# Kernel optimization log

Hardware: AMD Instinct MI355X
Metric: run time of the kernel (lower is better)

The kernel has to match this reference:

```python
import jax, jax.numpy as jnp
import numpy as np

C = 512
H = 8  # num_heads
GROUPS = 32
EPS = 1e-5


def group_norm(x, scale, bias):
    # x: [b, c, h, w]; GroupNorm(32, c) normalizes over (c//32, h, w) per group
    b, c, h, w = x.shape
    xg = x.reshape(b, GROUPS, c // GROUPS * h * w)
    mean = jnp.mean(xg, axis=-1, keepdims=True)
    var = jnp.var(xg, axis=-1, keepdims=True)
    xg = (xg - mean) * jax.lax.rsqrt(var + EPS)
    x = xg.reshape(b, c, h, w)
    return x * scale[None, :, None, None] + bias[None, :, None, None]


def setup_inputs() -> dict:
    key = jax.random.key(0)
    ks = jax.random.split(key, 6)
    init = 0.02
    return {
        "x": jax.random.normal(ks[0], (8, C, 32, 32), dtype=jnp.float32),
        "gn_scale": jnp.ones((C,), jnp.float32),
        "gn_bias": jnp.zeros((C,), jnp.float32),
        "Wq": jax.random.normal(ks[1], (C, C), jnp.float32) * init,
        "bq": jnp.zeros((C,), jnp.float32),
        "Wk": jax.random.normal(ks[2], (C, C), jnp.float32) * init,
        "bk": jnp.zeros((C,), jnp.float32),
        "Wv": jax.random.normal(ks[3], (C, C), jnp.float32) * init,
        "bv": jnp.zeros((C,), jnp.float32),
        "Wo": jax.random.normal(ks[4], (C, C), jnp.float32) * init,
        "bo": jnp.zeros((C,), jnp.float32),
    }


def reference(x, gn_scale, gn_bias, Wq, bq, Wk, bk, Wv, bv, Wo, bo):
    b, c, h, w = x.shape
    s = h * w  # number of spatial tokens
    d = c // H  # head dim
    residual = x
    xn = group_norm(x, gn_scale, gn_bias)
    t = xn.reshape(b, c, s).transpose(0, 2, 1)  # [b, s, c]
    # torch Linear: y = x @ W.T + b
    q = t @ Wq.T + bq
    k = t @ Wk.T + bk
    v = t @ Wv.T + bv
    q = q.reshape(b, s, H, d).transpose(0, 2, 1, 3)  # [b, H, s, d]
    k = k.reshape(b, s, H, d).transpose(0, 2, 1, 3)
    v = v.reshape(b, s, H, d).transpose(0, 2, 1, 3)
    scale = d ** -0.5
    attn = jnp.einsum('bhqd,bhkd->bhqk', q, k) * scale  # [b, H, s, s]
    attn = jax.nn.softmax(attn, axis=-1)
    out = jnp.einsum('bhqk,bhkd->bhqd', attn, v)  # [b, H, s, d]
    out = out.transpose(0, 2, 1, 3).reshape(b, s, c)
    out = out @ Wo.T + bo
    out = out.transpose(0, 2, 1).reshape(b, c, h, w)
    return out + residual
```

## Files before the change

kernel.cpp:

```cpp
#include <hip/hip_runtime.h>


typedef __bf16 bf16x8 __attribute__((ext_vector_type(8)));
typedef __bf16 bf16x4 __attribute__((ext_vector_type(4)));
typedef float floatx4 __attribute__((ext_vector_type(4)));

static __device__ __forceinline__ floatx4 mfma16(bf16x8 a, bf16x8 b, floatx4 c) {
  return __builtin_amdgcn_mfma_f32_16x16x32_bf16(a, b, c, 0, 0, 0);
}
static __device__ __forceinline__ floatx4 mfma_fp8(long a, long b, floatx4 c) {
  return __builtin_amdgcn_mfma_f32_16x16x32_fp8_fp8(a, b, c, 0, 0, 0);
}

static __device__ __forceinline__ void async_cp16(const void* g, void* l) {
  __builtin_amdgcn_global_load_lds(
      (const __attribute__((address_space(1))) unsigned int*)g,
      (__attribute__((address_space(3))) unsigned int*)l, 16, 0, 0);
}

static __device__ __forceinline__ uint2 cvt8_bf16_fp8(uint4 v) {
  union { uint4 u; __bf16 h[8]; } in; in.u = v;
  float f[8];
#pragma unroll
  for (int i = 0; i < 8; ++i) f[i] = (float)in.h[i];
  int lo = __builtin_amdgcn_cvt_pk_fp8_f32(f[0], f[1], 0, false);
  lo = __builtin_amdgcn_cvt_pk_fp8_f32(f[2], f[3], lo, true);
  int hi = __builtin_amdgcn_cvt_pk_fp8_f32(f[4], f[5], 0, false);
  hi = __builtin_amdgcn_cvt_pk_fp8_f32(f[6], f[7], hi, true);
  return uint2{(unsigned)lo, (unsigned)hi};
}

__global__ __launch_bounds__(256) void prep_gn_kernel(
    const float* __restrict__ x, const float* __restrict__ gamma,
    const float* __restrict__ beta,
    const float* __restrict__ Wq, const float* __restrict__ bq,
    const float* __restrict__ Wk, const float* __restrict__ bk,
    const float* __restrict__ Wv, const float* __restrict__ bv,
    const float* __restrict__ Wo,
    __bf16* __restrict__ wqkv, __bf16* __restrict__ wo,
    float* __restrict__ bqkv, __bf16* __restrict__ t) {
  __shared__ __bf16 tile[16 * 1024];
  __shared__ float rbuf[8];
  int tid = threadIdx.x;
  int bx = blockIdx.x;

  if (bx >= 256) {
    const float SC = 0.125f * 1.4426950408889634f;
    int i = ((bx - 256) * 256 + tid) * 4;
    float4 q4 = *(const float4*)(Wq + i);
    float4 k4 = *(const float4*)(Wk + i);
    float4 v4 = *(const float4*)(Wv + i);
    float4 o4 = *(const float4*)(Wo + i);
    *(bf16x4*)(wqkv + i) = (bf16x4){(__bf16)(q4.x * SC), (__bf16)(q4.y * SC),
                                    (__bf16)(q4.z * SC), (__bf16)(q4.w * SC)};
    *(bf16x4*)(wqkv + 262144 + i) =
        (bf16x4){(__bf16)k4.x, (__bf16)k4.y, (__bf16)k4.z, (__bf16)k4.w};
    *(bf16x4*)(wqkv + 524288 + i) =
        (bf16x4){(__bf16)v4.x, (__bf16)v4.y, (__bf16)v4.z, (__bf16)v4.w};
    *(bf16x4*)(wo + i) =
        (bf16x4){(__bf16)o4.x, (__bf16)o4.y, (__bf16)o4.z, (__bf16)o4.w};
    int j = (bx - 256) * 256 + tid;
    if (j < 512) {
      bqkv[j]        = bq[j] * SC;
      bqkv[512 + j]  = bk[j];
      bqkv[1024 + j] = bv[j];
    }
    return;
  }

  int b = bx >> 5, g = bx & 31;
  const float* xp = x + (size_t)(b * 512 + g * 16) * 1024;
  const float4* xp4 = (const float4*)xp;

  float sacc = 0.f, ssacc = 0.f;
#pragma unroll
  for (int it = 0; it < 16; ++it) {
    float4 v = xp4[it * 256 + tid];
    sacc += v.x + v.y + v.z + v.w;
    ssacc += v.x * v.x + v.y * v.y + v.z * v.z + v.w * v.w;
  }
#pragma unroll
  for (int off = 1; off < 64; off <<= 1) {
    sacc += __shfl_xor(sacc, off);
    ssacc += __shfl_xor(ssacc, off);
  }
  int wv = tid >> 6;
  if ((tid & 63) == 0) { rbuf[wv] = sacc; rbuf[4 + wv] = ssacc; }
  __syncthreads();
  float S1 = rbuf[0] + rbuf[1] + rbuf[2] + rbuf[3];
  float S2 = rbuf[4] + rbuf[5] + rbuf[6] + rbuf[7];
  float mean = S1 * (1.f / 16384.f);
  float var = S2 * (1.f / 16384.f) - mean * mean;
  float inv = rsqrtf(var + 1e-5f);

#pragma unroll
  for (int it = 0; it < 16; ++it) {
    float4 v = xp4[it * 256 + tid];
    float ga = gamma[g * 16 + it], be = beta[g * 16 + it];
    int base = it * 1024 + tid * 4;
    tile[base + 0] = (__bf16)((v.x - mean) * inv * ga + be);
    tile[base + 1] = (__bf16)((v.y - mean) * inv * ga + be);
    tile[base + 2] = (__bf16)((v.z - mean) * inv * ga + be);
    tile[base + 3] = (__bf16)((v.w - mean) * inv * ga + be);
  }
  __syncthreads();

#pragma unroll
  for (int j = 0; j < 8; ++j) {
    int qid = j * 256 + tid;
    int sidx = qid >> 1, half = qid & 1;
    union { uint4 u; __bf16 h[8]; } o;
#pragma unroll
    for (int i = 0; i < 8; ++i) o.h[i] = tile[(half * 8 + i) * 1024 + sidx];
    *(uint4*)(t + (size_t)(b * 1024 + sidx) * 512 + g * 16 + half * 8) = o.u;
  }
}

__global__ __launch_bounds__(256) void gemm_qkv_kernel(
    const __bf16* __restrict__ t, const __bf16* __restrict__ wqkv,
    const float* __restrict__ bqkv,
    unsigned char* __restrict__ qb, unsigned char* __restrict__ kb,
    unsigned char* __restrict__ vt) {
  __shared__ __align__(16) __bf16 smem[8192];
  __bf16* As = smem;
  __bf16* Bs = smem + 4096;
  int tid = threadIdx.x;
  int m0 = blockIdx.x * 128;
  int n0 = blockIdx.y * 128;
  int wave = tid >> 6, lane = tid & 63;
  int l15 = lane & 15, quad = lane >> 4;
  int wm = wave >> 1, wn = wave & 1;

  floatx4 acc[4][4];
#pragma unroll
  for (int mi = 0; mi < 4; ++mi)
#pragma unroll
    for (int ni = 0; ni < 4; ++ni) acc[mi][ni] = (floatx4){0.f, 0.f, 0.f, 0.f};

  int r1 = tid >> 2, o1 = (tid & 3) * 8;
  const __bf16* gA1 = t + (size_t)(m0 + r1) * 512 + o1;
  const __bf16* gA2 = t + (size_t)(m0 + 64 + r1) * 512 + o1;
  const __bf16* gB1 = wqkv + (size_t)(n0 + r1) * 512 + o1;
  const __bf16* gB2 = wqkv + (size_t)(n0 + 64 + r1) * 512 + o1;
  __bf16* lA1 = As + tid * 8;
  __bf16* lA2 = As + 2048 + tid * 8;
  __bf16* lB1 = Bs + tid * 8;
  __bf16* lB2 = Bs + 2048 + tid * 8;

  for (int k0 = 0; k0 < 512; k0 += 32) {
    async_cp16(gA1 + k0, lA1);
    async_cp16(gA2 + k0, lA2);
    async_cp16(gB1 + k0, lB1);
    async_cp16(gB2 + k0, lB2);
    __syncthreads();
    bf16x8 af[4], bfr[4];
#pragma unroll
    for (int mi = 0; mi < 4; ++mi)
      af[mi] = *(const bf16x8*)&As[(wm * 64 + mi * 16 + l15) * 32 + quad * 8];
#pragma unroll
    for (int ni = 0; ni < 4; ++ni)
      bfr[ni] = *(const bf16x8*)&Bs[(wn * 64 + ni * 16 + l15) * 32 + quad * 8];
#pragma unroll
    for (int mi = 0; mi < 4; ++mi)
#pragma unroll
      for (int ni = 0; ni < 4; ++ni)
        acc[mi][ni] = mfma16(af[mi], bfr[ni], acc[mi][ni]);
    __syncthreads();
  }

  int mat = n0 >> 9;
  int bidx = m0 >> 10, s0 = m0 & 1023;
  int hA = (n0 & 511) >> 6;
  float bias[4];
#pragma unroll
  for (int ni = 0; ni < 4; ++ni)
    bias[ni] = bqkv[n0 + wn * 64 + ni * 16 + l15];

  if (mat < 2) {
    unsigned char* dst = (mat == 0) ? qb : kb;
    for (int c = 0; c < 4; ++c) {
      if ((c >> 1) == wm) {
#pragma unroll
        for (int mi2 = 0; mi2 < 2; ++mi2) {
          int mi = (c & 1) * 2 + mi2;
          int lrow = mi2 * 16 + quad * 4;
#pragma unroll
          for (int ni = 0; ni < 4; ++ni)
#pragma unroll
            for (int r = 0; r < 4; ++r)
              smem[(lrow + r) * 136 + wn * 64 + ni * 16 + l15] =
                  (__bf16)(acc[mi][ni][r] + bias[ni]);
        }
      }
      __syncthreads();
#pragma unroll
      for (int u = 0; u < 2; ++u) {
        int f = tid * 16 + u * 8;
        int row = f >> 7, col = f & 127;
        uint2 val = cvt8_bf16_fp8(*(uint4*)&smem[row * 136 + col]);
        int head = hA + (col >> 6), d = col & 63;
        *(uint2*)(dst + ((size_t)(bidx * 8 + head) * 1024 + s0 + c * 32 + row) * 64 + d) = val;
      }
      __syncthreads();
    }
  } else {
    for (int c = 0; c < 4; ++c) {
      if ((c >> 1) == wn) {
#pragma unroll
        for (int ni2 = 0; ni2 < 2; ++ni2) {
          int ni = (c & 1) * 2 + ni2;
          int nrow = ni2 * 16 + l15;
#pragma unroll
          for (int mi = 0; mi < 4; ++mi)
#pragma unroll
            for (int r = 0; r < 4; ++r)
              smem[nrow * 136 + wm * 64 + mi * 16 + quad * 4 + r] =
                  (__bf16)(acc[mi][ni][r] + bias[ni]);
        }
      }
      __syncthreads();
#pragma unroll
      for (int u = 0; u < 2; ++u) {
        int f = tid * 16 + u * 8;
        int nrow = f >> 7, mcol = f & 127;
        uint2 val = cvt8_bf16_fp8(*(uint4*)&smem[nrow * 136 + mcol]);
        int nloc = c * 32 + nrow;
        int head = hA + (nloc >> 6), d = nloc & 63;
        *(uint2*)(vt + ((size_t)(bidx * 8 + head) * 64 + d) * 1024 + s0 + mcol) = val;
      }
      __syncthreads();
    }
  }
}

__global__ __launch_bounds__(256) void attn_kernel(
    const unsigned char* __restrict__ qb, const unsigned char* __restrict__ kb,
    const unsigned char* __restrict__ vt, __bf16* __restrict__ ao) {
  __shared__ __align__(16) unsigned char Ks[2][64 * 80];
  __shared__ __align__(16) unsigned char Vs[2][64 * 80];
  __shared__ __align__(16) __bf16 Ps[128 * 72];
  unsigned char* Psb = (unsigned char*)Ps;
  int tid = threadIdx.x;
  int bx = blockIdx.x;
  int b = bx >> 6, h = (bx >> 3) & 7, q128 = bx & 7;
  int wv = tid >> 6, lane = tid & 63, l15 = lane & 15, quad = lane >> 4;
  size_t bh = (size_t)(b * 8 + h) * 65536;
  const unsigned char* Qp = qb + bh;
  const unsigned char* Kp = kb + bh;
  const unsigned char* Vp = vt + bh;
  int q0 = q128 * 128, qw = q0 + wv * 32;

  long aq[2][2];
#pragma unroll
  for (int mi = 0; mi < 2; ++mi)
#pragma unroll
    for (int kh = 0; kh < 2; ++kh)
      aq[mi][kh] = *(const long*)(Qp + (size_t)(qw + mi * 16 + l15) * 64 + kh * 32 + quad * 8);

  const long ONES = 0x3838383838383838L;

  floatx4 oacc[2][4], lacc[2];
#pragma unroll
  for (int mi = 0; mi < 2; ++mi) {
    lacc[mi] = (floatx4){0.f, 0.f, 0.f, 0.f};
#pragma unroll
    for (int di = 0; di < 4; ++di) oacc[mi][di] = (floatx4){0.f, 0.f, 0.f, 0.f};
  }

  int srow = tid >> 2, scol = (tid & 3) * 16;
  int ldsoff = srow * 80 + scol;

  uint4 kr, vr;
  kr = *(const uint4*)(Kp + (size_t)srow * 64 + scol);
  vr = *(const uint4*)(Vp + (size_t)srow * 1024 + scol);

  for (int kt = 0; kt < 16; ++kt) {
    int cur = kt & 1;
    *(uint4*)&Ks[cur][ldsoff] = kr;
    *(uint4*)&Vs[cur][ldsoff] = vr;
    if (kt < 15) {
      int nt = kt + 1;
      kr = *(const uint4*)(Kp + (size_t)(nt * 64 + srow) * 64 + scol);
      vr = *(const uint4*)(Vp + (size_t)srow * 1024 + nt * 64 + scol);
    }
    __syncthreads();

    floatx4 sa[2][4];
#pragma unroll
    for (int ni = 0; ni < 4; ++ni) {
      long bk0 = *(const long*)&Ks[cur][(ni * 16 + l15) * 80 + quad * 8];
      long bk1 = *(const long*)&Ks[cur][(ni * 16 + l15) * 80 + 32 + quad * 8];
#pragma unroll
      for (int mi = 0; mi < 2; ++mi) {
        floatx4 s4 = (floatx4){0.f, 0.f, 0.f, 0.f};
        s4 = mfma_fp8(bk0, aq[mi][0], s4);
        s4 = mfma_fp8(bk1, aq[mi][1], s4);
        sa[mi][ni] = s4;
      }
    }

#pragma unroll
    for (int mi = 0; mi < 2; ++mi)
#pragma unroll
      for (int ni = 0; ni < 4; ++ni) {
        float e0 = __builtin_amdgcn_exp2f(sa[mi][ni][0]);
        float e1 = __builtin_amdgcn_exp2f(sa[mi][ni][1]);
        float e2 = __builtin_amdgcn_exp2f(sa[mi][ni][2]);
        float e3 = __builtin_amdgcn_exp2f(sa[mi][ni][3]);
        int pk = __builtin_amdgcn_cvt_pk_fp8_f32(e0, e1, 0, false);
        pk = __builtin_amdgcn_cvt_pk_fp8_f32(e2, e3, pk, true);
        *(unsigned int*)&Psb[(wv * 32 + mi * 16 + l15) * 72 + ni * 16 + quad * 4] =
            (unsigned)pk;
      }

    long ap[2][2];
#pragma unroll
    for (int mi = 0; mi < 2; ++mi) {
      ap[mi][0] = *(const long*)&Psb[(wv * 32 + mi * 16 + l15) * 72 + quad * 8];
      ap[mi][1] = *(const long*)&Psb[(wv * 32 + mi * 16 + l15) * 72 + 32 + quad * 8];
    }
#pragma unroll
    for (int di = 0; di < 4; ++di) {
      long bv0 = *(const long*)&Vs[cur][(di * 16 + l15) * 80 + quad * 8];
      long bv1 = *(const long*)&Vs[cur][(di * 16 + l15) * 80 + 32 + quad * 8];
#pragma unroll
      for (int mi = 0; mi < 2; ++mi) {
        oacc[mi][di] = mfma_fp8(ap[mi][0], bv0, oacc[mi][di]);
        oacc[mi][di] = mfma_fp8(ap[mi][1], bv1, oacc[mi][di]);
      }
    }
#pragma unroll
    for (int mi = 0; mi < 2; ++mi) {
      lacc[mi] = mfma_fp8(ap[mi][0], ONES, lacc[mi]);
      lacc[mi] = mfma_fp8(ap[mi][1], ONES, lacc[mi]);
    }
  }

  __syncthreads();
#pragma unroll
  for (int mi = 0; mi < 2; ++mi)
#pragma unroll
    for (int r = 0; r < 4; ++r) {
      float invl = 1.f / lacc[mi][r];
      int lrow = wv * 32 + mi * 16 + quad * 4 + r;
#pragma unroll
      for (int di = 0; di < 4; ++di)
        Ps[lrow * 72 + di * 16 + l15] = (__bf16)(oacc[mi][di][r] * invl);
    }
  __syncthreads();
  __bf16* aop = ao + (size_t)b * 524288 + h * 64;
#pragma unroll
  for (int u = 0; u < 4; ++u) {
    int idx = u * 256 + tid;
    int row = idx >> 3, col = (idx & 7) * 8;
    *(uint4*)(aop + (size_t)(q0 + row) * 512 + col) = *(uint4*)&Ps[row * 72 + col];
  }
}

__global__ __launch_bounds__(256) void gemm_out_kernel(
    const __bf16* __restrict__ ao, const __bf16* __restrict__ wo,
    const float* __restrict__ bo, const float* __restrict__ x,
    float* __restrict__ out) {
  __shared__ __align__(16) __bf16 As[128 * 32];
  __shared__ __align__(16) __bf16 Bs[64 * 32];
  __shared__ __align__(16) float ctile[32 * 132];
  int tid = threadIdx.x;
  int m0 = blockIdx.x * 128;
  int n0 = blockIdx.y * 64;
  int wave = tid >> 6, lane = tid & 63;
  int l15 = lane & 15, quad = lane >> 4;
  int wm = wave >> 1, wn = wave & 1;

  floatx4 acc[4][2];
#pragma unroll
  for (int mi = 0; mi < 4; ++mi)
#pragma unroll
    for (int ni = 0; ni < 2; ++ni) acc[mi][ni] = (floatx4){0.f, 0.f, 0.f, 0.f};

  int r1 = tid >> 2, o1 = (tid & 3) * 8;
  const __bf16* gA1 = ao + (size_t)(m0 + r1) * 512 + o1;
  const __bf16* gA2 = ao + (size_t)(m0 + 64 + r1) * 512 + o1;
  const __bf16* gB1 = wo + (size_t)(n0 + r1) * 512 + o1;
  __bf16* lA1 = As + tid * 8;
  __bf16* lA2 = As + 2048 + tid * 8;
  __bf16* lB1 = Bs + tid * 8;

  for (int k0 = 0; k0 < 512; k0 += 32) {
    async_cp16(gA1 + k0, lA1);
    async_cp16(gA2 + k0, lA2);
    async_cp16(gB1 + k0, lB1);
    __syncthreads();
    bf16x8 af[4], bfr[2];
#pragma unroll
    for (int mi = 0; mi < 4; ++mi)
      af[mi] = *(const bf16x8*)&As[(wm * 64 + mi * 16 + l15) * 32 + quad * 8];
#pragma unroll
    for (int ni = 0; ni < 2; ++ni)
      bfr[ni] = *(const bf16x8*)&Bs[(wn * 32 + ni * 16 + l15) * 32 + quad * 8];
#pragma unroll
    for (int mi = 0; mi < 4; ++mi)
#pragma unroll
      for (int ni = 0; ni < 2; ++ni)
        acc[mi][ni] = mfma16(af[mi], bfr[ni], acc[mi][ni]);
    __syncthreads();
  }

  int b = m0 >> 10, s0 = m0 & 1023;
  for (int cc = 0; cc < 2; ++cc) {
    __syncthreads();
    if (wn == cc) {
#pragma unroll
      for (int ni = 0; ni < 2; ++ni) {
        int nn = ni * 16 + l15;
        float bias = bo[n0 + cc * 32 + nn];
#pragma unroll
        for (int mi = 0; mi < 4; ++mi)
#pragma unroll
          for (int r = 0; r < 4; ++r)
            ctile[nn * 132 + wm * 64 + mi * 16 + quad * 4 + r] =
                acc[mi][ni][r] + bias;
      }
    }
    __syncthreads();
    int nn = tid >> 3, mlb = (tid & 7) * 16;
    int n = n0 + cc * 32 + nn;
    const float* xr = x + (size_t)(b * 512 + n) * 1024 + s0;
    float* orow = out + (size_t)(b * 512 + n) * 1024 + s0;
#pragma unroll
    for (int i = 0; i < 16; i += 4) {
      float4 cv = *(float4*)&ctile[nn * 132 + mlb + i];
      float4 xv = *(const float4*)&xr[mlb + i];
      float4 ov = {cv.x + xv.x, cv.y + xv.y, cv.z + xv.z, cv.w + xv.w};
      *(float4*)&orow[mlb + i] = ov;
    }
  }
}

extern "C" void kernel_launch(void* const* d_in, const int* in_sizes, int n_in,
                              void* d_out, int out_size, void* d_ws, size_t ws_size,
                              hipStream_t stream) {
  const float* x  = (const float*)d_in[0];
  const float* gs = (const float*)d_in[1];
  const float* gb = (const float*)d_in[2];
  const float* Wq = (const float*)d_in[3];
  const float* bq = (const float*)d_in[4];
  const float* Wk = (const float*)d_in[5];
  const float* bk = (const float*)d_in[6];
  const float* Wv = (const float*)d_in[7];
  const float* bv = (const float*)d_in[8];
  const float* Wo = (const float*)d_in[9];
  const float* bo = (const float*)d_in[10];
  float* out = (float*)d_out;

  char* ws = (char*)d_ws;
  __bf16* wqkv = (__bf16*)(ws);
  __bf16* wo   = (__bf16*)(ws + 1572864);
  float*  bqkv = (float*)(ws + 2097152);
  __bf16* t    = (__bf16*)(ws + 2103296);
  __bf16* ao   = t;
  unsigned char* qb = (unsigned char*)(ws + 10491904);
  unsigned char* kb = (unsigned char*)(ws + 14686208);
  unsigned char* vtb = (unsigned char*)(ws + 18880512);

  prep_gn_kernel<<<dim3(512), dim3(256), 0, stream>>>(
      x, gs, gb, Wq, bq, Wk, bk, Wv, bv, Wo, wqkv, wo, bqkv, t);
  gemm_qkv_kernel<<<dim3(64, 12), dim3(256), 0, stream>>>(t, wqkv, bqkv, qb, kb, vtb);
  attn_kernel<<<dim3(512), dim3(256), 0, stream>>>(qb, kb, vtb, ao);
  gemm_out_kernel<<<dim3(64, 8), dim3(256), 0, stream>>>(ao, wo, bo, x, out);
}
```

Before: 148.6 us.

## Switch QKV and output projection GEMMs to FP8 MFMA with swizzled LDS

Converts the normalized activations, the weights (scaled by 16) and the attention output to FP8, and runs both projection GEMMs with FP8 16x16x32 MFMA over a K-step of 64 using an XOR-swizzled LDS layout. The softmax scale moves from the Wq weights into the attention exp2 step, and the projection outputs are rescaled by 1/16 or 1/256. This halves the bytes moved for activations and weights and uses the faster FP8 matrix path, but adds more FP8 rounding error and extra conversion work in prep and attention.

Result: faster. 144.7 us (-2.7%).

```diff
diff --git a/kernel.cpp b/kernel.cpp
--- a/kernel.cpp
+++ b/kernel.cpp
@@ -5,9 +5,6 @@
 typedef __bf16 bf16x4 __attribute__((ext_vector_type(4)));
 typedef float floatx4 __attribute__((ext_vector_type(4)));
 
-static __device__ __forceinline__ floatx4 mfma16(bf16x8 a, bf16x8 b, floatx4 c) {
-  return __builtin_amdgcn_mfma_f32_16x16x32_bf16(a, b, c, 0, 0, 0);
-}
 static __device__ __forceinline__ floatx4 mfma_fp8(long a, long b, floatx4 c) {
   return __builtin_amdgcn_mfma_f32_16x16x32_fp8_fp8(a, b, c, 0, 0, 0);
 }
@@ -28,6 +25,14 @@
   int hi = __builtin_amdgcn_cvt_pk_fp8_f32(f[4], f[5], 0, false);
   hi = __builtin_amdgcn_cvt_pk_fp8_f32(f[6], f[7], hi, true);
   return uint2{(unsigned)lo, (unsigned)hi};
+}
+
+static __device__ __forceinline__ int swz_s(int r) {
+  return (r & 3) ^ ((r >> 2) & 3);
+}
+static __device__ __forceinline__ int frag_addr(int row, int kh, int quad) {
+  int chunk = (kh << 1) | (quad >> 1);
+  return row * 64 + ((chunk ^ swz_s(row)) << 4) + ((quad & 1) << 3);
 }
 
 __global__ __launch_bounds__(256) void prep_gn_kernel(
@@ -37,31 +42,35 @@
     const float* __restrict__ Wk, const float* __restrict__ bk,
     const float* __restrict__ Wv, const float* __restrict__ bv,
     const float* __restrict__ Wo,
-    __bf16* __restrict__ wqkv, __bf16* __restrict__ wo,
-    float* __restrict__ bqkv, __bf16* __restrict__ t) {
+    unsigned char* __restrict__ wqkv, unsigned char* __restrict__ wo,
+    float* __restrict__ bqkv, unsigned char* __restrict__ t) {
   __shared__ __bf16 tile[16 * 1024];
   __shared__ float rbuf[8];
   int tid = threadIdx.x;
   int bx = blockIdx.x;
 
   if (bx >= 256) {
-    const float SC = 0.125f * 1.4426950408889634f;
     int i = ((bx - 256) * 256 + tid) * 4;
     float4 q4 = *(const float4*)(Wq + i);
     float4 k4 = *(const float4*)(Wk + i);
     float4 v4 = *(const float4*)(Wv + i);
     float4 o4 = *(const float4*)(Wo + i);
-    *(bf16x4*)(wqkv + i) = (bf16x4){(__bf16)(q4.x * SC), (__bf16)(q4.y * SC),
-                                    (__bf16)(q4.z * SC), (__bf16)(q4.w * SC)};
-    *(bf16x4*)(wqkv + 262144 + i) =
-        (bf16x4){(__bf16)k4.x, (__bf16)k4.y, (__bf16)k4.z, (__bf16)k4.w};
-    *(bf16x4*)(wqkv + 524288 + i) =
-        (bf16x4){(__bf16)v4.x, (__bf16)v4.y, (__bf16)v4.z, (__bf16)v4.w};
-    *(bf16x4*)(wo + i) =
-        (bf16x4){(__bf16)o4.x, (__bf16)o4.y, (__bf16)o4.z, (__bf16)o4.w};
+    int p;
+    p = __builtin_amdgcn_cvt_pk_fp8_f32(q4.x * 16.f, q4.y * 16.f, 0, false);
+    p = __builtin_amdgcn_cvt_pk_fp8_f32(q4.z * 16.f, q4.w * 16.f, p, true);
+    *(unsigned int*)(wqkv + i) = (unsigned)p;
+    p = __builtin_amdgcn_cvt_pk_fp8_f32(k4.x * 16.f, k4.y * 16.f, 0, false);
+    p = __builtin_amdgcn_cvt_pk_fp8_f32(k4.z * 16.f, k4.w * 16.f, p, true);
+    *(unsigned int*)(wqkv + 262144 + i) = (unsigned)p;
+    p = __builtin_amdgcn_cvt_pk_fp8_f32(v4.x * 16.f, v4.y * 16.f, 0, false);
+    p = __builtin_amdgcn_cvt_pk_fp8_f32(v4.z * 16.f, v4.w * 16.f, p, true);
+    *(unsigned int*)(wqkv + 524288 + i) = (unsigned)p;
+    p = __builtin_amdgcn_cvt_pk_fp8_f32(o4.x * 16.f, o4.y * 16.f, 0, false);
+    p = __builtin_amdgcn_cvt_pk_fp8_f32(o4.z * 16.f, o4.w * 16.f, p, true);
+    *(unsigned int*)(wo + i) = (unsigned)p;
     int j = (bx - 256) * 256 + tid;
     if (j < 512) {
-      bqkv[j]        = bq[j] * SC;
+      bqkv[j]        = bq[j];
       bqkv[512 + j]  = bk[j];
       bqkv[1024 + j] = bv[j];
     }
@@ -112,18 +121,20 @@
     union { uint4 u; __bf16 h[8]; } o;
 #pragma unroll
     for (int i = 0; i < 8; ++i) o.h[i] = tile[(half * 8 + i) * 1024 + sidx];
-    *(uint4*)(t + (size_t)(b * 1024 + sidx) * 512 + g * 16 + half * 8) = o.u;
+    uint2 v8 = cvt8_bf16_fp8(o.u);
+    *(uint2*)(t + (size_t)(b * 1024 + sidx) * 512 + g * 16 + half * 8) = v8;
   }
 }
 
 __global__ __launch_bounds__(256) void gemm_qkv_kernel(
-    const __bf16* __restrict__ t, const __bf16* __restrict__ wqkv,
+    const unsigned char* __restrict__ t, const unsigned char* __restrict__ wqkv,
     const float* __restrict__ bqkv,
     unsigned char* __restrict__ qb, unsigned char* __restrict__ kb,
     unsigned char* __restrict__ vt) {
-  __shared__ __align__(16) __bf16 smem[8192];
-  __bf16* As = smem;
-  __bf16* Bs = smem + 4096;
+  __shared__ __align__(16) unsigned char smemraw[16384];
+  unsigned char* As = smemraw;
+  unsigned char* Bs = smemraw + 8192;
+  __bf16* ctile = (__bf16*)smemraw;
   int tid = threadIdx.x;
   int m0 = blockIdx.x * 128;
   int n0 = blockIdx.y * 128;
@@ -137,34 +148,40 @@
 #pragma unroll
     for (int ni = 0; ni < 4; ++ni) acc[mi][ni] = (floatx4){0.f, 0.f, 0.f, 0.f};
 
-  int r1 = tid >> 2, o1 = (tid & 3) * 8;
-  const __bf16* gA1 = t + (size_t)(m0 + r1) * 512 + o1;
-  const __bf16* gA2 = t + (size_t)(m0 + 64 + r1) * 512 + o1;
-  const __bf16* gB1 = wqkv + (size_t)(n0 + r1) * 512 + o1;
-  const __bf16* gB2 = wqkv + (size_t)(n0 + 64 + r1) * 512 + o1;
-  __bf16* lA1 = As + tid * 8;
-  __bf16* lA2 = As + 2048 + tid * 8;
-  __bf16* lB1 = Bs + tid * 8;
-  __bf16* lB2 = Bs + 2048 + tid * 8;
-
-  for (int k0 = 0; k0 < 512; k0 += 32) {
-    async_cp16(gA1 + k0, lA1);
-    async_cp16(gA2 + k0, lA2);
-    async_cp16(gB1 + k0, lB1);
-    async_cp16(gB2 + k0, lB2);
-    __syncthreads();
-    bf16x8 af[4], bfr[4];
-#pragma unroll
-    for (int mi = 0; mi < 4; ++mi)
-      af[mi] = *(const bf16x8*)&As[(wm * 64 + mi * 16 + l15) * 32 + quad * 8];
-#pragma unroll
-    for (int ni = 0; ni < 4; ++ni)
-      bfr[ni] = *(const bf16x8*)&Bs[(wn * 64 + ni * 16 + l15) * 32 + quad * 8];
-#pragma unroll
-    for (int mi = 0; mi < 4; ++mi)
+  const unsigned char* gA[2]; const unsigned char* gB[2];
+  unsigned char *lA[2], *lB[2];
+#pragma unroll
+  for (int u = 0; u < 2; ++u) {
+    int slot = u * 256 + tid;
+    int r = slot >> 2, cs = slot & 3;
+    int c = cs ^ swz_s(r);
+    gA[u] = t + (size_t)(m0 + r) * 512 + c * 16;
+    gB[u] = wqkv + (size_t)(n0 + r) * 512 + c * 16;
+    lA[u] = As + slot * 16;
+    lB[u] = Bs + slot * 16;
+  }
+
+  for (int k0 = 0; k0 < 512; k0 += 64) {
+    async_cp16(gA[0] + k0, lA[0]);
+    async_cp16(gA[1] + k0, lA[1]);
+    async_cp16(gB[0] + k0, lB[0]);
+    async_cp16(gB[1] + k0, lB[1]);
+    __syncthreads();
+#pragma unroll
+    for (int kh = 0; kh < 2; ++kh) {
+      long af[4], bfr[4];
+#pragma unroll
+      for (int mi = 0; mi < 4; ++mi)
+        af[mi] = *(const long*)&As[frag_addr(wm * 64 + mi * 16 + l15, kh, quad)];
 #pragma unroll
       for (int ni = 0; ni < 4; ++ni)
-        acc[mi][ni] = mfma16(af[mi], bfr[ni], acc[mi][ni]);
+        bfr[ni] = *(const long*)&Bs[frag_addr(wn * 64 + ni * 16 + l15, kh, quad)];
+#pragma unroll
+      for (int mi = 0; mi < 4; ++mi)
+#pragma unroll
+        for (int ni = 0; ni < 4; ++ni)
+          acc[mi][ni] = mfma_fp8(af[mi], bfr[ni], acc[mi][ni]);
+    }
     __syncthreads();
   }
 
@@ -188,8 +205,8 @@
           for (int ni = 0; ni < 4; ++ni)
 #pragma unroll
             for (int r = 0; r < 4; ++r)
-              smem[(lrow + r) * 136 + wn * 64 + ni * 16 + l15] =
-                  (__bf16)(acc[mi][ni][r] + bias[ni]);
+              ctile[(lrow + r) * 136 + wn * 64 + ni * 16 + l15] =
+                  (__bf16)(acc[mi][ni][r] * 0.0625f + bias[ni]);
         }
       }
       __syncthreads();
@@ -197,7 +214,7 @@
       for (int u = 0; u < 2; ++u) {
         int f = tid * 16 + u * 8;
         int row = f >> 7, col = f & 127;
-        uint2 val = cvt8_bf16_fp8(*(uint4*)&smem[row * 136 + col]);
+        uint2 val = cvt8_bf16_fp8(*(uint4*)&ctile[row * 136 + col]);
         int head = hA + (col >> 6), d = col & 63;
         *(uint2*)(dst + ((size_t)(bidx * 8 + head) * 1024 + s0 + c * 32 + row) * 64 + d) = val;
       }
@@ -214,8 +231,8 @@
           for (int mi = 0; mi < 4; ++mi)
 #pragma unroll
             for (int r = 0; r < 4; ++r)
-              smem[nrow * 136 + wm * 64 + mi * 16 + quad * 4 + r] =
-                  (__bf16)(acc[mi][ni][r] + bias[ni]);
+              ctile[nrow * 136 + wm * 64 + mi * 16 + quad * 4 + r] =
+                  (__bf16)(acc[mi][ni][r] * 0.0625f + bias[ni]);
         }
       }
       __syncthreads();
@@ -223,7 +240,7 @@
       for (int u = 0; u < 2; ++u) {
         int f = tid * 16 + u * 8;
         int nrow = f >> 7, mcol = f & 127;
-        uint2 val = cvt8_bf16_fp8(*(uint4*)&smem[nrow * 136 + mcol]);
+        uint2 val = cvt8_bf16_fp8(*(uint4*)&ctile[nrow * 136 + mcol]);
         int nloc = c * 32 + nrow;
         int head = hA + (nloc >> 6), d = nloc & 63;
         *(uint2*)(vt + ((size_t)(bidx * 8 + head) * 64 + d) * 1024 + s0 + mcol) = val;
@@ -235,11 +252,12 @@
 
 __global__ __launch_bounds__(256) void attn_kernel(
     const unsigned char* __restrict__ qb, const unsigned char* __restrict__ kb,
-    const unsigned char* __restrict__ vt, __bf16* __restrict__ ao) {
+    const unsigned char* __restrict__ vt, unsigned char* __restrict__ ao) {
   __shared__ __align__(16) unsigned char Ks[2][64 * 80];
   __shared__ __align__(16) unsigned char Vs[2][64 * 80];
   __shared__ __align__(16) __bf16 Ps[128 * 72];
   unsigned char* Psb = (unsigned char*)Ps;
+  const float SCL = 0.125f * 1.4426950408889634f;
   int tid = threadIdx.x;
   int bx = blockIdx.x;
   int b = bx >> 6, h = (bx >> 3) & 7, q128 = bx & 7;
@@ -303,10 +321,10 @@
     for (int mi = 0; mi < 2; ++mi)
 #pragma unroll
       for (int ni = 0; ni < 4; ++ni) {
-        float e0 = __builtin_amdgcn_exp2f(sa[mi][ni][0]);
-        float e1 = __builtin_amdgcn_exp2f(sa[mi][ni][1]);
-        float e2 = __builtin_amdgcn_exp2f(sa[mi][ni][2]);
-        float e3 = __builtin_amdgcn_exp2f(sa[mi][ni][3]);
+        float e0 = __builtin_amdgcn_exp2f(sa[mi][ni][0] * SCL);
+        float e1 = __builtin_amdgcn_exp2f(sa[mi][ni][1] * SCL);
+        float e2 = __builtin_amdgcn_exp2f(sa[mi][ni][2] * SCL);
+        float e3 = __builtin_amdgcn_exp2f(sa[mi][ni][3] * SCL);
         int pk = __builtin_amdgcn_cvt_pk_fp8_f32(e0, e1, 0, false);
         pk = __builtin_amdgcn_cvt_pk_fp8_f32(e2, e3, pk, true);
         *(unsigned int*)&Psb[(wv * 32 + mi * 16 + l15) * 72 + ni * 16 + quad * 4] =
@@ -341,28 +359,29 @@
   for (int mi = 0; mi < 2; ++mi)
 #pragma unroll
     for (int r = 0; r < 4; ++r) {
-      float invl = 1.f / lacc[mi][r];
+      float invl = 16.f / lacc[mi][r];
       int lrow = wv * 32 + mi * 16 + quad * 4 + r;
 #pragma unroll
       for (int di = 0; di < 4; ++di)
         Ps[lrow * 72 + di * 16 + l15] = (__bf16)(oacc[mi][di][r] * invl);
     }
   __syncthreads();
-  __bf16* aop = ao + (size_t)b * 524288 + h * 64;
+  unsigned char* aop = ao + (size_t)b * 524288 + h * 64;
 #pragma unroll
   for (int u = 0; u < 4; ++u) {
     int idx = u * 256 + tid;
     int row = idx >> 3, col = (idx & 7) * 8;
-    *(uint4*)(aop + (size_t)(q0 + row) * 512 + col) = *(uint4*)&Ps[row * 72 + col];
+    uint2 v8 = cvt8_bf16_fp8(*(uint4*)&Ps[row * 72 + col]);
+    *(uint2*)(aop + (size_t)(q0 + row) * 512 + col) = v8;
   }
 }
 
 __global__ __launch_bounds__(256) void gemm_out_kernel(
-    const __bf16* __restrict__ ao, const __bf16* __restrict__ wo,
+    const unsigned char* __restrict__ ao, const unsigned char* __restrict__ wo,
     const float* __restrict__ bo, const float* __restrict__ x,
     float* __restrict__ out) {
-  __shared__ __align__(16) __bf16 As[128 * 32];
-  __shared__ __align__(16) __bf16 Bs[64 * 32];
+  __shared__ __align__(16) unsigned char As[128 * 64];
+  __shared__ __align__(16) unsigned char Bs[64 * 64];
   __shared__ __align__(16) float ctile[32 * 132];
   int tid = threadIdx.x;
   int m0 = blockIdx.x * 128;
@@ -377,31 +396,43 @@
 #pragma unroll
     for (int ni = 0; ni < 2; ++ni) acc[mi][ni] = (floatx4){0.f, 0.f, 0.f, 0.f};
 
-  int r1 = tid >> 2, o1 = (tid & 3) * 8;
-  const __bf16* gA1 = ao + (size_t)(m0 + r1) * 512 + o1;
-  const __bf16* gA2 = ao + (size_t)(m0 + 64 + r1) * 512 + o1;
-  const __bf16* gB1 = wo + (size_t)(n0 + r1) * 512 + o1;
-  __bf16* lA1 = As + tid * 8;
-  __bf16* lA2 = As + 2048 + tid * 8;
-  __bf16* lB1 = Bs + tid * 8;
-
-  for (int k0 = 0; k0 < 512; k0 += 32) {
-    async_cp16(gA1 + k0, lA1);
-    async_cp16(gA2 + k0, lA2);
+  const unsigned char* gA[2]; unsigned char* lA[2];
+#pragma unroll
+  for (int u = 0; u < 2; ++u) {
+    int slot = u * 256 + tid;
+    int r = slot >> 2, cs = slot & 3;
+    int c = cs ^ swz_s(r);
+    gA[u] = ao + (size_t)(m0 + r) * 512 + c * 16;
+    lA[u] = As + slot * 16;
+  }
+  const unsigned char* gB1; unsigned char* lB1;
+  {
+    int r = tid >> 2, cs = tid & 3;
+    int c = cs ^ swz_s(r);
+    gB1 = wo + (size_t)(n0 + r) * 512 + c * 16;
+    lB1 = Bs + tid * 16;
+  }
+
+  for (int k0 = 0; k0 < 512; k0 += 64) {
+    async_cp16(gA[0] + k0, lA[0]);
+    async_cp16(gA[1] + k0, lA[1]);
     async_cp16(gB1 + k0, lB1);
     __syncthreads();
-    bf16x8 af[4], bfr[2];
-#pragma unroll
-    for (int mi = 0; mi < 4; ++mi)
-      af[mi] = *(const bf16x8*)&As[(wm * 64 + mi * 16 + l15) * 32 + quad * 8];
-#pragma unroll
-    for (int ni = 0; ni < 2; ++ni)
-      bfr[ni] = *(const bf16x8*)&Bs[(wn * 32 + ni * 16 + l15) * 32 + quad * 8];
-#pragma unroll
-    for (int mi = 0; mi < 4; ++mi)
+#pragma unroll
+    for (int kh = 0; kh < 2; ++kh) {
+      long af[4], bfr[2];
+#pragma unroll
+      for (int mi = 0; mi < 4; ++mi)
+        af[mi] = *(const long*)&As[frag_addr(wm * 64 + mi * 16 + l15, kh, quad)];
 #pragma unroll
       for (int ni = 0; ni < 2; ++ni)
-        acc[mi][ni] = mfma16(af[mi], bfr[ni], acc[mi][ni]);
+        bfr[ni] = *(const long*)&Bs[frag_addr(wn * 32 + ni * 16 + l15, kh, quad)];
+#pragma unroll
+      for (int mi = 0; mi < 4; ++mi)
+#pragma unroll
+        for (int ni = 0; ni < 2; ++ni)
+          acc[mi][ni] = mfma_fp8(af[mi], bfr[ni], acc[mi][ni]);
+    }
     __syncthreads();
   }
 
@@ -418,7 +449,7 @@
 #pragma unroll
           for (int r = 0; r < 4; ++r)
             ctile[nn * 132 + wm * 64 + mi * 16 + quad * 4 + r] =
-                acc[mi][ni][r] + bias;
+                acc[mi][ni][r] * (1.f / 256.f) + bias;
       }
     }
     __syncthreads();
@@ -453,14 +484,14 @@
   float* out = (float*)d_out;
 
   char* ws = (char*)d_ws;
-  __bf16* wqkv = (__bf16*)(ws);
-  __bf16* wo   = (__bf16*)(ws + 1572864);
-  float*  bqkv = (float*)(ws + 2097152);
-  __bf16* t    = (__bf16*)(ws + 2103296);
-  __bf16* ao   = t;
-  unsigned char* qb = (unsigned char*)(ws + 10491904);
-  unsigned char* kb = (unsigned char*)(ws + 14686208);
-  unsigned char* vtb = (unsigned char*)(ws + 18880512);
+  unsigned char* wqkv = (unsigned char*)(ws);
+  unsigned char* wo   = (unsigned char*)(ws + 786432);
+  float* bqkv = (float*)(ws + 1048576);
+  unsigned char* t    = (unsigned char*)(ws + 1054720);
+  unsigned char* ao   = t;
+  unsigned char* qb   = (unsigned char*)(ws + 5249024);
+  unsigned char* kb   = (unsigned char*)(ws + 9443328);
+  unsigned char* vtb  = (unsigned char*)(ws + 13637632);
 
   prep_gn_kernel<<<dim3(512), dim3(256), 0, stream>>>(
       x, gs, gb, Wq, bq, Wk, bk, Wv, bv, Wo, wqkv, wo, bqkv, t);
```
